# Kernel tuning notes

Measured on AMD Instinct MI355X. Metric: run time of the kernel, lower is better.

The kernel has to match this reference:

```python
import jax, jax.numpy as jnp
import numpy as np

N = 8192
F = 64
OUT = 64


def setup_inputs() -> dict:
    key = jax.random.key(0)
    k1, k2, k3 = jax.random.split(key, 3)
    adj = jax.random.uniform(k1, (N, N), dtype=jnp.float32)
    features = jax.random.normal(k2, (N, F), dtype=jnp.float32)
    # torch Linear weight: [out_features, in_features*2], xavier_uniform with relu gain
    gain = float(np.sqrt(2.0))
    fan_in, fan_out = 2 * F, OUT
    bound = gain * float(np.sqrt(6.0 / (fan_in + fan_out)))
    W = jax.random.uniform(k3, (OUT, 2 * F), dtype=jnp.float32, minval=-bound, maxval=bound)
    return {"adj": adj, "features": features, "W": W}


def reference(adj, features, W):
    # neigh = (adj @ x) / (rowsum(adj) + 1)   -- dense 2D branch of SageConvLayer
    deg = jnp.sum(adj, axis=1, keepdims=True) + 1.0          # [N, 1]
    neigh = jnp.matmul(adj, features) / deg                   # [N, F]
    data = jnp.concatenate([features, neigh], axis=-1)        # [N, 2F]
    return jnp.matmul(data, W.T)                              # [N, OUT]
```

## Files before the change

kernel.cpp:

```cpp
#include <hip/hip_runtime.h>

#define NN 8192
#define FF 64
#define NOUT 64
#define KS 8
#define KCHUNK (NN / KS)
#define MROWS 64

typedef __bf16 bf16x8 __attribute__((ext_vector_type(8)));
typedef float f32x4 __attribute__((ext_vector_type(4)));

__device__ inline bf16x8 cvt8(f32x4 a, f32x4 b) {
    bf16x8 r;
    #pragma unroll
    for (int i = 0; i < 4; ++i) { r[i] = (__bf16)a[i]; r[i + 4] = (__bf16)b[i]; }
    return r;
}

__global__ __launch_bounds__(256)
void transpose_kernel(const float* __restrict__ feat, __bf16* __restrict__ featT) {
    __shared__ __bf16 t[64][72];
    int tid = threadIdx.x;
    int n0 = blockIdx.x * 64;
    {
        int r = tid >> 2, cg = (tid & 3) * 16;
        const float* p = feat + (size_t)(n0 + r) * FF + cg;
        f32x4 v0 = *(const f32x4*)(p);
        f32x4 v1 = *(const f32x4*)(p + 4);
        f32x4 v2 = *(const f32x4*)(p + 8);
        f32x4 v3 = *(const f32x4*)(p + 12);
        #pragma unroll
        for (int j = 0; j < 4; ++j) {
            t[r][cg + 0 + j]  = (__bf16)v0[j];
            t[r][cg + 4 + j]  = (__bf16)v1[j];
            t[r][cg + 8 + j]  = (__bf16)v2[j];
            t[r][cg + 12 + j] = (__bf16)v3[j];
        }
    }
    __syncthreads();
    int f = tid >> 2, seg = (tid & 3) * 16;
    bf16x8 o0, o1;
    #pragma unroll
    for (int i = 0; i < 8; ++i) { o0[i] = t[seg + i][f]; o1[i] = t[seg + 8 + i][f]; }
    *(bf16x8*)&featT[(size_t)f * NN + n0 + seg]     = o0;
    *(bf16x8*)&featT[(size_t)f * NN + n0 + seg + 8] = o1;
}

__global__ __launch_bounds__(256, 4)
void main_kernel(const float* __restrict__ adj, const __bf16* __restrict__ featT,
                 __bf16* __restrict__ partN, float* __restrict__ partDeg) {
    int tid = threadIdx.x;
    int w = tid >> 6, lane = tid & 63, ln = lane & 15, q = lane >> 4;
    int ks = blockIdx.x & (KS - 1);
    int mt = blockIdx.x >> 3;

    int rowA = mt * MROWS + w * 16 + ln;
    const float* ap = adj + (size_t)rowA * NN + (size_t)ks * KCHUNK + q * 8;
    const __bf16* bbase = featT + (size_t)ln * NN + (size_t)ks * KCHUNK + q * 8;
    const __bf16* bp0 = bbase;
    const __bf16* bp1 = bbase + (size_t)16 * NN;
    const __bf16* bp2 = bbase + (size_t)32 * NN;
    const __bf16* bp3 = bbase + (size_t)48 * NN;

    f32x4 acc[4], accd;
    accd = 0;
    #pragma unroll
    for (int t = 0; t < 4; ++t) acc[t] = 0;

    bf16x8 ones;
    __bf16 o = (ln == 0) ? (__bf16)1.0f : (__bf16)0.0f;
    #pragma unroll
    for (int i = 0; i < 8; ++i) ones[i] = o;

    #pragma unroll 2
    for (int s = 0; s < KCHUNK / 32; ++s) {
        f32x4 a0 = __builtin_nontemporal_load((const f32x4*)(ap + s * 32));
        f32x4 a1 = __builtin_nontemporal_load((const f32x4*)(ap + s * 32 + 4));
        bf16x8 b0 = *(const bf16x8*)(bp0 + s * 32);
        bf16x8 b1 = *(const bf16x8*)(bp1 + s * 32);
        bf16x8 b2 = *(const bf16x8*)(bp2 + s * 32);
        bf16x8 b3 = *(const bf16x8*)(bp3 + s * 32);
        bf16x8 af = cvt8(a0, a1);
        acc[0] = __builtin_amdgcn_mfma_f32_16x16x32_bf16(af, b0, acc[0], 0, 0, 0);
        acc[1] = __builtin_amdgcn_mfma_f32_16x16x32_bf16(af, b1, acc[1], 0, 0, 0);
        acc[2] = __builtin_amdgcn_mfma_f32_16x16x32_bf16(af, b2, acc[2], 0, 0, 0);
        acc[3] = __builtin_amdgcn_mfma_f32_16x16x32_bf16(af, b3, acc[3], 0, 0, 0);
        accd   = __builtin_amdgcn_mfma_f32_16x16x32_bf16(af, ones, accd, 0, 0, 0);
    }

    int grow = mt * MROWS + w * 16 + q * 4;
    #pragma unroll
    for (int r = 0; r < 4; ++r) {
        size_t base = ((size_t)(ks << 13) + grow + r) * FF + ln;
        partN[base +  0] = (__bf16)acc[0][r];
        partN[base + 16] = (__bf16)acc[1][r];
        partN[base + 32] = (__bf16)acc[2][r];
        partN[base + 48] = (__bf16)acc[3][r];
    }
    if (ln == 0) {
        #pragma unroll
        for (int r = 0; r < 4; ++r)
            partDeg[(ks << 13) + grow + r] = accd[r];
    }
}

__global__ __launch_bounds__(256)
void epilogue_kernel(const float* __restrict__ feat, const float* __restrict__ W,
                     const __bf16* __restrict__ partN, const float* __restrict__ partDeg,
                     float* __restrict__ out) {
    __shared__ __bf16 dataB[64][136];
    __shared__ float rdeg[64];
    int tid = threadIdx.x, blk = blockIdx.x;

    if (tid < 64) {
        float s = 0.f;
        #pragma unroll
        for (int ks = 0; ks < KS; ++ks) s += partDeg[(ks << 13) + blk * 64 + tid];
        rdeg[tid] = 1.0f / (s + 1.0f);
    }
    __syncthreads();

    #pragma unroll
    for (int i = 0; i < 2; ++i) {
        int idx = tid + i * 256;
        int r = idx >> 3, c = (idx & 7) * 8;
        float s[8];
        #pragma unroll
        for (int j = 0; j < 8; ++j) s[j] = 0.f;
        #pragma unroll
        for (int ks = 0; ks < KS; ++ks) {
            bf16x8 v = *(const bf16x8*)&partN[((size_t)(ks << 13) + blk * 64 + r) * FF + c];
            #pragma unroll
            for (int j = 0; j < 8; ++j) s[j] += (float)v[j];
        }
        float rd = rdeg[r];
        bf16x8 o;
        #pragma unroll
        for (int j = 0; j < 8; ++j) o[j] = (__bf16)(s[j] * rd);
        *(bf16x8*)&dataB[r][64 + c] = o;
    }
    #pragma unroll
    for (int i = 0; i < 2; ++i) {
        int idx = tid + i * 256;
        int r = idx >> 3, c = (idx & 7) * 8;
        const float* p = feat + (size_t)(blk * 64 + r) * FF + c;
        f32x4 f0 = *(const f32x4*)p;
        f32x4 f1 = *(const f32x4*)(p + 4);
        *(bf16x8*)&dataB[r][c] = cvt8(f0, f1);
    }
    __syncthreads();

    int w = tid >> 6, lane = tid & 63, ln = lane & 15, q = lane >> 4;
    f32x4 acc[4];
    #pragma unroll
    for (int t = 0; t < 4; ++t) acc[t] = 0;

    #pragma unroll
    for (int kk = 0; kk < 4; ++kk) {
        bf16x8 af = *(const bf16x8*)&dataB[w * 16 + ln][kk * 32 + q * 8];
        #pragma unroll
        for (int t = 0; t < 4; ++t) {
            const float* wp = W + (size_t)(t * 16 + ln) * 128 + kk * 32 + q * 8;
            f32x4 b0 = *(const f32x4*)wp;
            f32x4 b1 = *(const f32x4*)(wp + 4);
            bf16x8 bf = cvt8(b0, b1);
            acc[t] = __builtin_amdgcn_mfma_f32_16x16x32_bf16(af, bf, acc[t], 0, 0, 0);
        }
    }

    int grow = blk * 64 + w * 16 + q * 4;
    #pragma unroll
    for (int t = 0; t < 4; ++t)
        #pragma unroll
        for (int r = 0; r < 4; ++r)
            out[(size_t)(grow + r) * NOUT + t * 16 + ln] = acc[t][r];
}

extern "C" void kernel_launch(void* const* d_in, const int* in_sizes, int n_in,
                              void* d_out, int out_size, void* d_ws, size_t ws_size,
                              hipStream_t stream) {
    const float* adj  = (const float*)d_in[0];
    const float* feat = (const float*)d_in[1];
    const float* W    = (const float*)d_in[2];
    float* out = (float*)d_out;
    char* ws = (char*)d_ws;

    __bf16* partN   = (__bf16*)ws;
    float*  partDeg = (float*)(ws + (size_t)KS * NN * FF * 2);
    __bf16* featT   = (__bf16*)(ws + (size_t)KS * NN * FF * 2 + (size_t)KS * NN * 4);

    transpose_kernel<<<NN / 64, 256, 0, stream>>>(feat, featT);
    main_kernel<<<(NN / MROWS) * KS, 256, 0, stream>>>(adj, featT, partN, partDeg);
    epilogue_kernel<<<NN / 64, 256, 0, stream>>>(feat, W, partN, partDeg, out);
}
```

Before: 408.4 us.

## Stage feature tiles in double-buffered swizzled LDS shared across waves

The B operand (transposed bf16 features) is now loaded cooperatively by the block into a double-buffered LDS tile with an XOR swizzle, instead of each wave loading it directly from global memory. The four waves share one copy, which cuts redundant global and L2 traffic, and the next tile is prefetched into registers while MFMAs run on the current one. In exchange the kernel uses 32 KB of LDS per block, which may limit occupancy at 4 blocks per CU, and adds a block barrier per tile. The kernel is likely bound by streaming adj, so the gain may be limited.

```diff
diff --git a/kernel.cpp b/kernel.cpp
--- a/kernel.cpp
+++ b/kernel.cpp
@@ -6,6 +6,9 @@
 #define KS 8
 #define KCHUNK (NN / KS)
 #define MROWS 64
+#define TILE_K 128
+#define NTILES (KCHUNK / TILE_K)
+#define BUFB (64 * TILE_K * 2)
 
 typedef __bf16 bf16x8 __attribute__((ext_vector_type(8)));
 typedef float f32x4 __attribute__((ext_vector_type(4)));
@@ -49,18 +52,23 @@
 __global__ __launch_bounds__(256, 4)
 void main_kernel(const float* __restrict__ adj, const __bf16* __restrict__ featT,
                  __bf16* __restrict__ partN, float* __restrict__ partDeg) {
+    __shared__ __bf16 bt[2][64 * TILE_K];
     int tid = threadIdx.x;
     int w = tid >> 6, lane = tid & 63, ln = lane & 15, q = lane >> 4;
     int ks = blockIdx.x & (KS - 1);
     int mt = blockIdx.x >> 3;
 
+    int sr = tid >> 2;
+    int scb = (tid & 3) * 4;
+    const __bf16* sp = featT + (size_t)sr * NN + (size_t)ks * KCHUNK;
+    char* swb = (char*)&bt[0][0];
+    int swoff[4];
+    #pragma unroll
+    for (int j = 0; j < 4; ++j)
+        swoff[j] = sr * 256 + (((scb + j) ^ (sr & 7)) * 16);
+
     int rowA = mt * MROWS + w * 16 + ln;
     const float* ap = adj + (size_t)rowA * NN + (size_t)ks * KCHUNK + q * 8;
-    const __bf16* bbase = featT + (size_t)ln * NN + (size_t)ks * KCHUNK + q * 8;
-    const __bf16* bp0 = bbase;
-    const __bf16* bp1 = bbase + (size_t)16 * NN;
-    const __bf16* bp2 = bbase + (size_t)32 * NN;
-    const __bf16* bp3 = bbase + (size_t)48 * NN;
 
     f32x4 acc[4], accd;
     accd = 0;
@@ -72,20 +80,47 @@
     #pragma unroll
     for (int i = 0; i < 8; ++i) ones[i] = o;
 
-    #pragma unroll 2
-    for (int s = 0; s < KCHUNK / 32; ++s) {
-        f32x4 a0 = __builtin_nontemporal_load((const f32x4*)(ap + s * 32));
-        f32x4 a1 = __builtin_nontemporal_load((const f32x4*)(ap + s * 32 + 4));
-        bf16x8 b0 = *(const bf16x8*)(bp0 + s * 32);
-        bf16x8 b1 = *(const bf16x8*)(bp1 + s * 32);
-        bf16x8 b2 = *(const bf16x8*)(bp2 + s * 32);
-        bf16x8 b3 = *(const bf16x8*)(bp3 + s * 32);
-        bf16x8 af = cvt8(a0, a1);
-        acc[0] = __builtin_amdgcn_mfma_f32_16x16x32_bf16(af, b0, acc[0], 0, 0, 0);
-        acc[1] = __builtin_amdgcn_mfma_f32_16x16x32_bf16(af, b1, acc[1], 0, 0, 0);
-        acc[2] = __builtin_amdgcn_mfma_f32_16x16x32_bf16(af, b2, acc[2], 0, 0, 0);
-        acc[3] = __builtin_amdgcn_mfma_f32_16x16x32_bf16(af, b3, acc[3], 0, 0, 0);
-        accd   = __builtin_amdgcn_mfma_f32_16x16x32_bf16(af, ones, accd, 0, 0, 0);
+    int rbase0 = (ln +  0) * 256, rbase1 = (ln + 16) * 256;
+    int rbase2 = (ln + 32) * 256, rbase3 = (ln + 48) * 256;
+    int lx = ln & 7;
+
+    bf16x8 stg[4];
+    #pragma unroll
+    for (int j = 0; j < 4; ++j) stg[j] = *(const bf16x8*)(sp + (scb + j) * 8);
+    #pragma unroll
+    for (int j = 0; j < 4; ++j) *(bf16x8*)(swb + swoff[j]) = stg[j];
+    __syncthreads();
+
+    for (int t = 0; t < NTILES; ++t) {
+        if (t + 1 < NTILES) {
+            #pragma unroll
+            for (int j = 0; j < 4; ++j)
+                stg[j] = *(const bf16x8*)(sp + (t + 1) * TILE_K + (scb + j) * 8);
+        }
+        const char* rb = (const char*)&bt[0][0] + (t & 1) * BUFB;
+        const float* at = ap + t * TILE_K;
+        #pragma unroll
+        for (int s = 0; s < 4; ++s) {
+            f32x4 a0 = __builtin_nontemporal_load((const f32x4*)(at + s * 32));
+            f32x4 a1 = __builtin_nontemporal_load((const f32x4*)(at + s * 32 + 4));
+            int blk = ((s * 4 + q) ^ lx) * 16;
+            bf16x8 b0 = *(const bf16x8*)(rb + rbase0 + blk);
+            bf16x8 b1 = *(const bf16x8*)(rb + rbase1 + blk);
+            bf16x8 b2 = *(const bf16x8*)(rb + rbase2 + blk);
+            bf16x8 b3 = *(const bf16x8*)(rb + rbase3 + blk);
+            bf16x8 af = cvt8(a0, a1);
+            acc[0] = __builtin_amdgcn_mfma_f32_16x16x32_bf16(af, b0, acc[0], 0, 0, 0);
+            acc[1] = __builtin_amdgcn_mfma_f32_16x16x32_bf16(af, b1, acc[1], 0, 0, 0);
+            acc[2] = __builtin_amdgcn_mfma_f32_16x16x32_bf16(af, b2, acc[2], 0, 0, 0);
+            acc[3] = __builtin_amdgcn_mfma_f32_16x16x32_bf16(af, b3, acc[3], 0, 0, 0);
+            accd   = __builtin_amdgcn_mfma_f32_16x16x32_bf16(af, ones, accd, 0, 0, 0);
+        }
+        if (t + 1 < NTILES) {
+            char* wb = swb + ((t + 1) & 1) * BUFB;
+            #pragma unroll
+            for (int j = 0; j < 4; ++j) *(bf16x8*)(wb + swoff[j]) = stg[j];
+            __syncthreads();
+        }
     }
 
     int grow = mt * MROWS + w * 16 + q * 4;
```

Result: faster. 375.2 us (-8.1%).
